# Kernel tuning notes

Hardware: AMD Instinct MI355X
Metric: run time of the kernel (lower is better)

## Reference

```python
import jax, jax.numpy as jnp
import numpy as np

T, B, F, H, O = 2048, 256, 64, 256, 1

def setup_inputs() -> dict:
    key = jax.random.key(0)
    k0, k1, k2 = jax.random.split(key, 3)
    return {
        "x": jax.random.normal(k0, (T, B, F), jnp.float32),          # (Time, Batch, Feat)
        "W0": jax.random.normal(k1, (H, F + H), jnp.float32) * 0.05,  # i2h weight (PyTorch layout)
        "b0": jnp.zeros((H,), jnp.float32),
        "Wfc": jax.random.normal(k2, (O, H), jnp.float32) * 0.05,     # fc1 weight
        "bfc": jnp.zeros((O,), jnp.float32),
        "feature_n": 0,
    }

def reference(x, W0, b0, Wfc, bfc, feature_n):
    # RnnCell: h = tanh(Linear(cat([x_t, h], 1))); then out_t = fc1(h).
    batch = x.shape[1]
    hidden = W0.shape[0]
    h0 = jnp.zeros((batch, hidden), x.dtype)

    def step(h, x_t):
        combined = jnp.concatenate([x_t, h], axis=1)          # (B, F+H)
        h_new = jnp.tanh(combined @ W0.T + b0)                # (B, H)
        out = h_new @ Wfc.T + bfc                             # (B, O)
        return h_new, out

    _, outs = jax.lax.scan(step, h0, x)                       # (T, B, O)
    # torch.stack(outputs, 1).squeeze(2) -> (B, T)
    return jnp.transpose(outs, (1, 0, 2)).squeeze(2)
```

## Files before the change

### kernel.cpp

```cpp
#include <hip/hip_runtime.h>

#define T_STEPS 2048
#define BATCH   256
#define FEAT    64
#define HID     256
#define KAUG    320
#define NW      8
#define NTHR    512
#define XTILE   16

typedef _Float16 half8 __attribute__((ext_vector_type(8)));
typedef float    f32x4 __attribute__((ext_vector_type(4)));
typedef float    f32x8 __attribute__((ext_vector_type(8)));

__device__ __forceinline__ float fast_tanh(float z) {
    float e = __expf(2.0f * z);
    return 1.0f - 2.0f * __builtin_amdgcn_rcpf(e + 1.0f);
}

__global__
__attribute__((amdgpu_flat_work_group_size(NTHR, NTHR), amdgpu_waves_per_eu(2, 2)))
void rnn_kernel(const float* __restrict__ x,
                const float* __restrict__ W0,
                const float* __restrict__ b0,
                const float* __restrict__ Wfc,
                const float* __restrict__ bfc,
                float* __restrict__ out)
{
    const int b    = blockIdx.x;
    const int tid  = threadIdx.x;
    const int w    = tid >> 6;
    const int lane = tid & 63;
    const int l15  = lane & 15;
    const int kg   = lane >> 4;

    __shared__ __align__(16) _Float16 h_buf[2][HID];
    __shared__ __align__(16) _Float16 x_tile[2][XTILE][FEAT];
    __shared__ __align__(16) float    out_buf[T_STEPS];

    half8 bw[2][10];
#pragma unroll
    for (int nt = 0; nt < 2; ++nt) {
        const int n = (2 * w + nt) * 16 + l15;
        const float* wp = W0 + n * KAUG + kg * 8;
#pragma unroll
        for (int c = 0; c < 10; ++c) {
            const f32x8 v = *reinterpret_cast<const f32x8*>(wp + c * 32);
            bw[nt][c] = __builtin_convertvector(v, half8);
        }
    }

    const float b00 = b0[32 * w + l15];
    const float b01 = b0[32 * w + 16 + l15];
    const float wf0 = Wfc[32 * w + l15];
    const float wf1 = Wfc[32 * w + 16 + l15];
    const float bfc_r = bfc[0];

    if (tid < HID) { h_buf[0][tid] = (_Float16)0.f; h_buf[1][tid] = (_Float16)0.f; }
#pragma unroll
    for (int i = 0; i < 4; ++i) out_buf[tid + i * NTHR] = bfc_r;

    const int tr = tid >> 5;
    const int f2 = (tid & 31) * 2;
    {
        const float2 v = *reinterpret_cast<const float2*>(
            x + (size_t)tr * (BATCH * FEAT) + b * FEAT + f2);
        union { _Float16 h[2]; unsigned u; } pk;
        pk.h[0] = (_Float16)v.x; pk.h[1] = (_Float16)v.y;
        *reinterpret_cast<unsigned*>(&x_tile[0][tr][f2]) = pk.u;
    }
    __syncthreads();

    for (int t = 0; t < T_STEPS; ++t) {
        const int cur = t & 1;
        const int nxt = cur ^ 1;
        const int xb  = (t >> 4) & 1;

        const bool do_stage = ((t & 15) == 0) && (t + XTILE < T_STEPS);
        float2 xld;
        if (do_stage) {
            xld = *reinterpret_cast<const float2*>(
                x + (size_t)(t + XTILE + tr) * (BATCH * FEAT) + b * FEAT + f2);
        }

        const _Float16* xrow = &x_tile[xb][t & 15][kg * 8];
        const _Float16* hrow = &h_buf[cur][kg * 8];

        f32x4 acc0a = {0.f, 0.f, 0.f, 0.f}, acc0b = {0.f, 0.f, 0.f, 0.f};
        f32x4 acc1a = {0.f, 0.f, 0.f, 0.f}, acc1b = {0.f, 0.f, 0.f, 0.f};
#pragma unroll
        for (int c = 0; c < 2; ++c) {
            const half8 af = *reinterpret_cast<const half8*>(xrow + c * 32);
            if (c & 1) {
                acc0b = __builtin_amdgcn_mfma_f32_16x16x32_f16(af, bw[0][c], acc0b, 0, 0, 0);
                acc1b = __builtin_amdgcn_mfma_f32_16x16x32_f16(af, bw[1][c], acc1b, 0, 0, 0);
            } else {
                acc0a = __builtin_amdgcn_mfma_f32_16x16x32_f16(af, bw[0][c], acc0a, 0, 0, 0);
                acc1a = __builtin_amdgcn_mfma_f32_16x16x32_f16(af, bw[1][c], acc1a, 0, 0, 0);
            }
        }
#pragma unroll
        for (int c = 2; c < 10; ++c) {
            const half8 af = *reinterpret_cast<const half8*>(hrow + (c - 2) * 32);
            if (c & 1) {
                acc0b = __builtin_amdgcn_mfma_f32_16x16x32_f16(af, bw[0][c], acc0b, 0, 0, 0);
                acc1b = __builtin_amdgcn_mfma_f32_16x16x32_f16(af, bw[1][c], acc1b, 0, 0, 0);
            } else {
                acc0a = __builtin_amdgcn_mfma_f32_16x16x32_f16(af, bw[0][c], acc0a, 0, 0, 0);
                acc1a = __builtin_amdgcn_mfma_f32_16x16x32_f16(af, bw[1][c], acc1a, 0, 0, 0);
            }
        }

        if (do_stage) {
            union { _Float16 h[2]; unsigned u; } pk;
            pk.h[0] = (_Float16)xld.x; pk.h[1] = (_Float16)xld.y;
            *reinterpret_cast<unsigned*>(&x_tile[xb ^ 1][tr][f2]) = pk.u;
        }

        if (lane < 16) {
            const float h0 = fast_tanh(acc0a[0] + acc0b[0] + b00);
            const float h1 = fast_tanh(acc1a[0] + acc1b[0] + b01);
            h_buf[nxt][32 * w + l15]      = (_Float16)h0;
            h_buf[nxt][32 * w + 16 + l15] = (_Float16)h1;

            float p = fmaf(wf0, h0, wf1 * h1);
#pragma unroll
            for (int m = 1; m <= 8; m <<= 1) p += __shfl_xor(p, m, 64);
            if (lane == 0) atomicAdd(&out_buf[t], p);
        }
        __syncthreads();
    }

    f32x4* o4 = reinterpret_cast<f32x4*>(out + b * T_STEPS);
    const f32x4* s4 = reinterpret_cast<const f32x4*>(out_buf);
    o4[tid] = s4[tid];
}

extern "C" void kernel_launch(void* const* d_in, const int* in_sizes, int n_in,
                              void* d_out, int out_size, void* d_ws, size_t ws_size,
                              hipStream_t stream) {
    const float* x   = (const float*)d_in[0];
    const float* W0  = (const float*)d_in[1];
    const float* b0  = (const float*)d_in[2];
    const float* Wfc = (const float*)d_in[3];
    const float* bfc = (const float*)d_in[4];
    float* out = (float*)d_out;

    rnn_kernel<<<dim3(BATCH), dim3(NTHR), 0, stream>>>(x, W0, b0, Wfc, bfc, out);
}
```

Before: 1.673 ms.

## Halve waves per batch row, defer fc reduction, replace atomics with per-wave partials

Moves from 8 waves to 4 waves per block, with each wave computing four 16-column tiles of the hidden state. This cuts the cost of the per-step barrier while putting more MFMAs in each wave. The fc1 output reduction is deferred by one step so its shuffles overlap the next step's MFMAs. The shared atomicAdd is replaced by per-wave partial buffers that are summed at the end. The A-fragment loads are limited to lane 0 of each 16-lane group, since only row 0 of the result is used, and x staging is widened to float4. The risks are fewer concurrent waves to hide latency and higher register pressure from the 40 weight fragments held per wave.

```diff
diff --git a/kernel.cpp b/kernel.cpp
--- a/kernel.cpp
+++ b/kernel.cpp
@@ -5,11 +5,12 @@
 #define FEAT    64
 #define HID     256
 #define KAUG    320
-#define NW      8
-#define NTHR    512
+#define NW      4
+#define NTHR    256
 #define XTILE   16
 
 typedef _Float16 half8 __attribute__((ext_vector_type(8)));
+typedef _Float16 half4 __attribute__((ext_vector_type(4)));
 typedef float    f32x4 __attribute__((ext_vector_type(4)));
 typedef float    f32x8 __attribute__((ext_vector_type(8)));
 
@@ -19,7 +20,7 @@
 }
 
 __global__
-__attribute__((amdgpu_flat_work_group_size(NTHR, NTHR), amdgpu_waves_per_eu(2, 2)))
+__attribute__((amdgpu_flat_work_group_size(NTHR, NTHR), amdgpu_waves_per_eu(1, 1)))
 void rnn_kernel(const float* __restrict__ x,
                 const float* __restrict__ W0,
                 const float* __restrict__ b0,
@@ -33,43 +34,49 @@
     const int lane = tid & 63;
     const int l15  = lane & 15;
     const int kg   = lane >> 4;
+    const bool alane = (l15 == 0);
 
     __shared__ __align__(16) _Float16 h_buf[2][HID];
     __shared__ __align__(16) _Float16 x_tile[2][XTILE][FEAT];
-    __shared__ __align__(16) float    out_buf[T_STEPS];
+    __shared__ __align__(16) float    out_part[NW][T_STEPS];
 
-    half8 bw[2][10];
+    half8 bw[4][10];
 #pragma unroll
-    for (int nt = 0; nt < 2; ++nt) {
-        const int n = (2 * w + nt) * 16 + l15;
+    for (int j = 0; j < 4; ++j) {
+        const int n = (4 * w + j) * 16 + l15;
         const float* wp = W0 + n * KAUG + kg * 8;
 #pragma unroll
         for (int c = 0; c < 10; ++c) {
             const f32x8 v = *reinterpret_cast<const f32x8*>(wp + c * 32);
-            bw[nt][c] = __builtin_convertvector(v, half8);
+            bw[j][c] = __builtin_convertvector(v, half8);
         }
     }
 
-    const float b00 = b0[32 * w + l15];
-    const float b01 = b0[32 * w + 16 + l15];
-    const float wf0 = Wfc[32 * w + l15];
-    const float wf1 = Wfc[32 * w + 16 + l15];
-    const float bfc_r = bfc[0];
+    float b0e[4] = {}, wfe[4] = {};
+    if (lane < 16) {
+#pragma unroll
+        for (int j = 0; j < 4; ++j) {
+            b0e[j] = b0[(4 * w + j) * 16 + lane];
+            wfe[j] = Wfc[(4 * w + j) * 16 + lane];
+        }
+    }
 
     if (tid < HID) { h_buf[0][tid] = (_Float16)0.f; h_buf[1][tid] = (_Float16)0.f; }
-#pragma unroll
-    for (int i = 0; i < 4; ++i) out_buf[tid + i * NTHR] = bfc_r;
-
-    const int tr = tid >> 5;
-    const int f2 = (tid & 31) * 2;
     {
-        const float2 v = *reinterpret_cast<const float2*>(
-            x + (size_t)tr * (BATCH * FEAT) + b * FEAT + f2);
-        union { _Float16 h[2]; unsigned u; } pk;
-        pk.h[0] = (_Float16)v.x; pk.h[1] = (_Float16)v.y;
-        *reinterpret_cast<unsigned*>(&x_tile[0][tr][f2]) = pk.u;
+        const int tr = tid >> 4, f4 = (tid & 15) * 4;
+        const f32x4 v = *reinterpret_cast<const f32x4*>(
+            x + (size_t)tr * (BATCH * FEAT) + b * FEAT + f4);
+        const half4 hv = {(_Float16)v.x, (_Float16)v.y, (_Float16)v.z, (_Float16)v.w};
+        *reinterpret_cast<half4*>(&x_tile[0][tr][f4]) = hv;
     }
     __syncthreads();
+
+    half8 af[10];
+#pragma unroll
+    for (int c = 0; c < 10; ++c) af[c] = half8{};
+
+    float p_prev = 0.f;
+    const f32x4 zero4 = {0.f, 0.f, 0.f, 0.f};
 
     for (int t = 0; t < T_STEPS; ++t) {
         const int cur = t & 1;
@@ -77,63 +84,86 @@
         const int xb  = (t >> 4) & 1;
 
         const bool do_stage = ((t & 15) == 0) && (t + XTILE < T_STEPS);
-        float2 xld;
+        const int tr = tid >> 4, f4 = (tid & 15) * 4;
+        f32x4 xld = zero4;
         if (do_stage) {
-            xld = *reinterpret_cast<const float2*>(
-                x + (size_t)(t + XTILE + tr) * (BATCH * FEAT) + b * FEAT + f2);
+            xld = *reinterpret_cast<const f32x4*>(
+                x + (size_t)(t + XTILE + tr) * (BATCH * FEAT) + b * FEAT + f4);
         }
 
-        const _Float16* xrow = &x_tile[xb][t & 15][kg * 8];
-        const _Float16* hrow = &h_buf[cur][kg * 8];
+        if (alane) {
+            af[0] = *reinterpret_cast<const half8*>(&x_tile[xb][t & 15][kg * 8]);
+            af[1] = *reinterpret_cast<const half8*>(&x_tile[xb][t & 15][32 + kg * 8]);
+#pragma unroll
+            for (int c = 2; c < 10; ++c)
+                af[c] = *reinterpret_cast<const half8*>(&h_buf[cur][(c - 2) * 32 + kg * 8]);
+        }
 
-        f32x4 acc0a = {0.f, 0.f, 0.f, 0.f}, acc0b = {0.f, 0.f, 0.f, 0.f};
-        f32x4 acc1a = {0.f, 0.f, 0.f, 0.f}, acc1b = {0.f, 0.f, 0.f, 0.f};
+        {
+            float p = p_prev;
+            p += __shfl_xor(p, 1, 64);
+            p += __shfl_xor(p, 2, 64);
+            p += __shfl_xor(p, 4, 64);
+            p += __shfl_xor(p, 8, 64);
+            if (lane == 0) out_part[w][(t + T_STEPS - 1) & (T_STEPS - 1)] = p;
+        }
+
+        f32x4 aE[4], aO[4];
 #pragma unroll
-        for (int c = 0; c < 2; ++c) {
-            const half8 af = *reinterpret_cast<const half8*>(xrow + c * 32);
-            if (c & 1) {
-                acc0b = __builtin_amdgcn_mfma_f32_16x16x32_f16(af, bw[0][c], acc0b, 0, 0, 0);
-                acc1b = __builtin_amdgcn_mfma_f32_16x16x32_f16(af, bw[1][c], acc1b, 0, 0, 0);
-            } else {
-                acc0a = __builtin_amdgcn_mfma_f32_16x16x32_f16(af, bw[0][c], acc0a, 0, 0, 0);
-                acc1a = __builtin_amdgcn_mfma_f32_16x16x32_f16(af, bw[1][c], acc1a, 0, 0, 0);
-            }
+        for (int j = 0; j < 4; ++j) {
+            aE[j] = __builtin_amdgcn_mfma_f32_16x16x32_f16(af[0], bw[j][0], zero4, 0, 0, 0);
+            aO[j] = __builtin_amdgcn_mfma_f32_16x16x32_f16(af[1], bw[j][1], zero4, 0, 0, 0);
         }
 #pragma unroll
-        for (int c = 2; c < 10; ++c) {
-            const half8 af = *reinterpret_cast<const half8*>(hrow + (c - 2) * 32);
-            if (c & 1) {
-                acc0b = __builtin_amdgcn_mfma_f32_16x16x32_f16(af, bw[0][c], acc0b, 0, 0, 0);
-                acc1b = __builtin_amdgcn_mfma_f32_16x16x32_f16(af, bw[1][c], acc1b, 0, 0, 0);
-            } else {
-                acc0a = __builtin_amdgcn_mfma_f32_16x16x32_f16(af, bw[0][c], acc0a, 0, 0, 0);
-                acc1a = __builtin_amdgcn_mfma_f32_16x16x32_f16(af, bw[1][c], acc1a, 0, 0, 0);
+        for (int c = 2; c < 10; c += 2) {
+#pragma unroll
+            for (int j = 0; j < 4; ++j) {
+                aE[j] = __builtin_amdgcn_mfma_f32_16x16x32_f16(af[c],     bw[j][c],     aE[j], 0, 0, 0);
+                aO[j] = __builtin_amdgcn_mfma_f32_16x16x32_f16(af[c + 1], bw[j][c + 1], aO[j], 0, 0, 0);
             }
         }
 
         if (do_stage) {
-            union { _Float16 h[2]; unsigned u; } pk;
-            pk.h[0] = (_Float16)xld.x; pk.h[1] = (_Float16)xld.y;
-            *reinterpret_cast<unsigned*>(&x_tile[xb ^ 1][tr][f2]) = pk.u;
+            const half4 hv = {(_Float16)xld.x, (_Float16)xld.y,
+                              (_Float16)xld.z, (_Float16)xld.w};
+            *reinterpret_cast<half4*>(&x_tile[xb ^ 1][tr][f4]) = hv;
         }
 
+        float pnew = 0.f;
         if (lane < 16) {
-            const float h0 = fast_tanh(acc0a[0] + acc0b[0] + b00);
-            const float h1 = fast_tanh(acc1a[0] + acc1b[0] + b01);
-            h_buf[nxt][32 * w + l15]      = (_Float16)h0;
-            h_buf[nxt][32 * w + 16 + l15] = (_Float16)h1;
+#pragma unroll
+            for (int j = 0; j < 4; ++j) {
+                const float z = aE[j][0] + aO[j][0] + b0e[j];
+                const float h = fast_tanh(z);
+                pnew = fmaf(wfe[j], h, pnew);
+                h_buf[nxt][(4 * w + j) * 16 + lane] = (_Float16)h;
+            }
+        }
+        p_prev = pnew;
 
-            float p = fmaf(wf0, h0, wf1 * h1);
-#pragma unroll
-            for (int m = 1; m <= 8; m <<= 1) p += __shfl_xor(p, m, 64);
-            if (lane == 0) atomicAdd(&out_buf[t], p);
-        }
         __syncthreads();
     }
 
-    f32x4* o4 = reinterpret_cast<f32x4*>(out + b * T_STEPS);
-    const f32x4* s4 = reinterpret_cast<const f32x4*>(out_buf);
-    o4[tid] = s4[tid];
+    {
+        float p = p_prev;
+        p += __shfl_xor(p, 1, 64);
+        p += __shfl_xor(p, 2, 64);
+        p += __shfl_xor(p, 4, 64);
+        p += __shfl_xor(p, 8, 64);
+        if (lane == 0) out_part[w][T_STEPS - 1] = p;
+    }
+    __syncthreads();
+
+    const float bfc_r = bfc[0];
+#pragma unroll
+    for (int i = 0; i < 2; ++i) {
+        const int t0 = tid * 8 + i * 4;
+        f32x4 s = {bfc_r, bfc_r, bfc_r, bfc_r};
+#pragma unroll
+        for (int ww = 0; ww < NW; ++ww)
+            s += *reinterpret_cast<const f32x4*>(&out_part[ww][t0]);
+        *reinterpret_cast<f32x4*>(out + b * T_STEPS + t0) = s;
+    }
 }
 
 extern "C" void kernel_launch(void* const* d_in, const int* in_sizes, int n_in,
```

Measured after the change: 1.727 ms. +3.3%, slower.
